# Optimization experiments

Hardware: AMD Instinct MI355X
Metric: run time of the kernel (lower is better)

## Reference

```python
import jax, jax.numpy as jnp
import numpy as np

B, N, D = 16, 1024, 768
H = 12
HD = D // H
HID = 4 * D
EPS = 1e-6


def _layernorm(x, g, b):
    mu = jnp.mean(x, axis=-1, keepdims=True)
    var = jnp.mean(jnp.square(x - mu), axis=-1, keepdims=True)
    return (x - mu) * jax.lax.rsqrt(var + EPS) * g + b


def setup_inputs() -> dict:
    key = jax.random.key(0)
    ks = jax.random.split(key, 8)
    s_d = 1.0 / np.sqrt(D)
    s_h = 1.0 / np.sqrt(HID)
    return {
        "x": jax.random.normal(ks[0], (B, N, D), dtype=jnp.float32),
        "qkv_w": jax.random.uniform(ks[1], (3 * D, D), jnp.float32, -s_d, s_d),
        "proj_w": jax.random.uniform(ks[2], (D, D), jnp.float32, -s_d, s_d),
        "proj_b": jax.random.uniform(ks[3], (D,), jnp.float32, -s_d, s_d),
        "fc1_w": jax.random.uniform(ks[4], (HID, D), jnp.float32, -s_d, s_d),
        "fc1_b": jax.random.uniform(ks[5], (HID,), jnp.float32, -s_d, s_d),
        "fc2_w": jax.random.uniform(ks[6], (D, HID), jnp.float32, -s_h, s_h),
        "fc2_b": jax.random.uniform(ks[7], (D,), jnp.float32, -s_h, s_h),
        "norm1_g": jnp.ones((D,), jnp.float32),
        "norm1_b": jnp.zeros((D,), jnp.float32),
        "norm2_g": jnp.ones((D,), jnp.float32),
        "norm2_b": jnp.zeros((D,), jnp.float32),
    }


def _attention(x, qkv_w, proj_w, proj_b):
    b, n, _ = x.shape
    qkv = x @ qkv_w.T                                  # [b,n,3D] (no bias: qkv_bias=False)
    qkv = qkv.reshape(b, n, 3, H, HD)
    q, k, v = (jnp.transpose(qkv[:, :, i], (0, 2, 1, 3)) for i in range(3))  # [b,h,n,hd]
    scale = HD ** (-0.5)
    dots = jnp.einsum("bhid,bhjd->bhij", q, k) * scale
    attn = jax.nn.softmax(dots, axis=-1)
    out = jnp.einsum("bhij,bhjd->bhid", attn, v)
    out = jnp.transpose(out, (0, 2, 1, 3)).reshape(b, n, H * HD)
    return out @ proj_w.T + proj_b


def _mlp(x, fc1_w, fc1_b, fc2_w, fc2_b):
    h = jax.nn.gelu(x @ fc1_w.T + fc1_b, approximate=False)
    return h @ fc2_w.T + fc2_b


def reference(x, qkv_w, proj_w, proj_b, fc1_w, fc1_b, fc2_w, fc2_b,
              norm1_g, norm1_b, norm2_g, norm2_b):
    x = x + _attention(_layernorm(x, norm1_g, norm1_b), qkv_w, proj_w, proj_b)
    x = x + _mlp(_layernorm(x, norm2_g, norm2_b), fc1_w, fc1_b, fc2_w, fc2_b)
    return x
```

## Files before the change

### kernel.cpp

```cpp
#include <hip/hip_runtime.h>
#include <hip/hip_bf16.h>
#include <math.h>

using bf16 = __hip_bfloat16;
typedef __attribute__((ext_vector_type(8))) short short8;
typedef __attribute__((ext_vector_type(4))) short shortx4;
typedef __attribute__((ext_vector_type(4))) float floatx4;

#define BB 16
#define NN 1024
#define DD 768
#define HH 12
#define HD 64
#define HID 3072

__device__ __forceinline__ floatx4 mfma_bf16(short8 a, short8 b, floatx4 c) {
  return __builtin_amdgcn_mfma_f32_16x16x32_bf16(a, b, c, 0, 0, 0);
}

__device__ __forceinline__ short bf16_bits(float f) {
  union { bf16 h; short s; } u;
  u.h = __float2bfloat16(f);
  return u.s;
}

__device__ __forceinline__ void async_copy16(const void* g, void* l) {
  __builtin_amdgcn_global_load_lds(
      (const __attribute__((address_space(1))) unsigned int*)g,
      (__attribute__((address_space(3))) unsigned int*)l,
      16, 0, 0);
}

__device__ __forceinline__ float gelu_f(float x) {
  const float z = x * fmaf(0.10294324f, x * x, 2.3022082f);
  const float e = exp2f(z);
  return x - x * __builtin_amdgcn_rcpf(e + 1.0f);
}

__global__ __launch_bounds__(256)
void cvt_kernel(const float* __restrict__ in, bf16* __restrict__ out, int n4)
{
  const int i = blockIdx.x * 256 + threadIdx.x;
  if (i >= n4) return;
  const float4 v = ((const float4*)in)[i];
  shortx4 o;
  o.x = bf16_bits(v.x); o.y = bf16_bits(v.y);
  o.z = bf16_bits(v.z); o.w = bf16_bits(v.w);
  ((shortx4*)out)[i] = o;
}

__global__ __launch_bounds__(256)
void ln_kernel(const float* __restrict__ x, const float* __restrict__ g,
               const float* __restrict__ b, bf16* __restrict__ y)
{
  const int row = blockIdx.x;
  const int t = threadIdx.x;
  const float* xr = x + (size_t)row * DD;
  float v[3];
  float s = 0.f, s2 = 0.f;
#pragma unroll
  for (int i = 0; i < 3; ++i) {
    float f = xr[t + i * 256];
    v[i] = f;
    s += f;
    s2 += f * f;
  }
#pragma unroll
  for (int off = 1; off < 64; off <<= 1) {
    s  += __shfl_xor(s, off);
    s2 += __shfl_xor(s2, off);
  }
  __shared__ float red[2][4];
  const int wave = t >> 6, lane = t & 63;
  if (lane == 0) { red[0][wave] = s; red[1][wave] = s2; }
  __syncthreads();
  s  = red[0][0] + red[0][1] + red[0][2] + red[0][3];
  s2 = red[1][0] + red[1][1] + red[1][2] + red[1][3];
  const float mu = s * (1.f / DD);
  const float var = s2 * (1.f / DD) - mu * mu;
  const float inv = rsqrtf(var + 1e-6f);
  bf16* yr = y + (size_t)row * DD;
#pragma unroll
  for (int i = 0; i < 3; ++i) {
    int c = t + i * 256;
    yr[c] = __float2bfloat16((v[i] - mu) * inv * g[c] + b[c]);
  }
}

template <int EPI>
__global__ __launch_bounds__(256, 4)
void gemm_kernel(const bf16* __restrict__ A, const bf16* __restrict__ W,
                 const float* __restrict__ bias, const float* __restrict__ res,
                 void* __restrict__ Cv, int N, int K)
{
  __shared__ __align__(16) short smem[16896];
  short* sA = smem;
  short* sB = smem + 8192;

  const int tid  = threadIdx.x;
  const int lane = tid & 63;
  const int wave = tid >> 6;
  const int wm = wave & 1, wn = wave >> 1;
  const int row16 = lane & 15, quad = lane >> 4;

  const int lin = blockIdx.y * gridDim.x + blockIdx.x;
  const int per = gridDim.x * 8;
  const int pan = lin / per, rem = lin % per;
  const int bm = (pan * 8 + (rem & 7)) * 128;
  const int bn = (rem >> 3) * 128;

  const int lrow = lane >> 3;
  const int lkc  = (lane & 7) ^ lrow;

  const bf16* Ag = A + (size_t)(bm + wave * 32 + lrow) * K + lkc * 8;
  const bf16* Bg = W + (size_t)(bn + wave * 32 + lrow) * K + lkc * 8;
  short* sAw = sA + wave * 2048;
  short* sBw = sB + wave * 2048;

  floatx4 acc[4][4] = {};

  for (int kt = 0; kt < K; kt += 64) {
#pragma unroll
    for (int g = 0; g < 4; ++g) {
      async_copy16(Ag + (size_t)g * 8 * K + kt, sAw + g * 512);
      async_copy16(Bg + (size_t)g * 8 * K + kt, sBw + g * 512);
    }
    __syncthreads();
#pragma unroll
    for (int c = 0; c < 2; ++c) {
      short8 af[4], bfr[4];
      const int kc = c * 4 + quad;
#pragma unroll
      for (int mt = 0; mt < 4; ++mt) {
        const int row = wm * 64 + mt * 16 + row16;
        af[mt] = *(const short8*)&sA[(row >> 3) * 512 + ((row & 7) * 8 + (kc ^ (row & 7))) * 8];
      }
#pragma unroll
      for (int nt = 0; nt < 4; ++nt) {
        const int row = wn * 64 + nt * 16 + row16;
        bfr[nt] = *(const short8*)&sB[(row >> 3) * 512 + ((row & 7) * 8 + (kc ^ (row & 7))) * 8];
      }
#pragma unroll
      for (int mt = 0; mt < 4; ++mt)
#pragma unroll
        for (int nt = 0; nt < 4; ++nt)
          acc[mt][nt] = mfma_bf16(bfr[nt], af[mt], acc[mt][nt]);
    }
    __syncthreads();
  }

  if (EPI == 1) {
#pragma unroll
    for (int mt = 0; mt < 4; ++mt) {
      const int row = bm + wm * 64 + mt * 16 + row16;
#pragma unroll
      for (int nt = 0; nt < 4; ++nt) {
        const int col = bn + wn * 64 + nt * 16 + quad * 4;
        const floatx4 bv = *(const floatx4*)&bias[col];
        const floatx4 rv = *(const floatx4*)&res[(size_t)row * N + col];
        floatx4 o;
#pragma unroll
        for (int r = 0; r < 4; ++r) o[r] = acc[mt][nt][r] + bv[r] + rv[r];
        *(floatx4*)&((float*)Cv)[(size_t)row * N + col] = o;
      }
    }
  } else {
    short* sC = smem;
#pragma unroll
    for (int mt = 0; mt < 4; ++mt) {
      const int lr = wm * 64 + mt * 16 + row16;
#pragma unroll
      for (int nt = 0; nt < 4; ++nt) {
        const int lc = wn * 64 + nt * 16 + quad * 4;
        floatx4 bv = {};
        if (EPI == 2) bv = *(const floatx4*)&bias[bn + lc];
        shortx4 pk;
#pragma unroll
        for (int r = 0; r < 4; ++r) {
          float v = acc[mt][nt][r] + bv[r];
          if (EPI == 2) v = gelu_f(v);
          pk[r] = bf16_bits(v);
        }
        *(shortx4*)&sC[lr * 132 + lc] = pk;
      }
    }
    __syncthreads();
#pragma unroll
    for (int it = 0; it < 8; ++it) {
      const int row = (tid >> 4) + it * 16;
      const int col = (tid & 15) * 8;
      short8 v = *(const short8*)&sC[row * 132 + col];
      *(short8*)&((bf16*)Cv)[(size_t)(bm + row) * N + bn + col] = v;
    }
  }
}

__global__ __launch_bounds__(256)
void vtrans_kernel(const bf16* __restrict__ qkv, bf16* __restrict__ vt)
{
  const int bh = blockIdx.y;
  const int b = bh / HH, h = bh % HH;
  const int n0 = blockIdx.x * 64;
  __shared__ __align__(16) short tile[64 * 72];
  const int tid = threadIdx.x;

  const int r = tid >> 2, c16 = (tid & 3) * 16;
  const bf16* src = qkv + (size_t)(b * NN + n0 + r) * 2304 + 2 * DD + h * 64 + c16;
  *(short8*)&tile[r * 72 + c16]     = *(const short8*)(src);
  *(short8*)&tile[r * 72 + c16 + 8] = *(const short8*)(src + 8);
  __syncthreads();

#pragma unroll
  for (int it = 0; it < 2; ++it) {
    const int d  = (tid >> 3) + it * 32;
    const int jg = (tid & 7) * 8;
    short8 o;
#pragma unroll
    for (int t = 0; t < 8; ++t) ((short*)&o)[t] = tile[(jg + t) * 72 + d];
    *(short8*)&vt[((size_t)bh * 64 + d) * NN + n0 + jg] = o;
  }
}

__global__ __launch_bounds__(256, 2)
void attn_kernel(const bf16* __restrict__ qkv, const bf16* __restrict__ vt,
                 bf16* __restrict__ out)
{
  const int bh = blockIdx.y;
  const int b = bh / HH, h = bh % HH;
  const int q0 = blockIdx.x * 128;
  const int tid = threadIdx.x;
  const int lane = tid & 63;
  const int wave = tid >> 6;
  const int row16 = lane & 15, quad = lane >> 4;

  __shared__ __align__(16) short sK[4096];
  __shared__ __align__(16) short sVt[4096];
  __shared__ __align__(16) short sP[4][2][1024];

  const bf16* base  = qkv + (size_t)b * NN * 2304 + h * 64;
  const bf16* vbase = vt + (size_t)bh * 64 * NN;

  short8 qf[2][2];
#pragma unroll
  for (int qg = 0; qg < 2; ++qg) {
    const bf16* qrow = base + (size_t)(q0 + wave * 32 + qg * 16 + row16) * 2304;
    qf[qg][0] = *(const short8*)(qrow + quad * 8);
    qf[qg][1] = *(const short8*)(qrow + 32 + quad * 8);
  }

  floatx4 o_acc[2][4] = {};
  floatx4 l_acc[2] = {};
  const short8 ones = { (short)0x3F80, (short)0x3F80, (short)0x3F80, (short)0x3F80,
                        (short)0x3F80, (short)0x3F80, (short)0x3F80, (short)0x3F80 };

  const bf16* ksrc = base + DD + (size_t)(wave * 16 + row16) * 2304 + quad * 8;
  const bf16* vsrc = vbase + (size_t)(wave * 16 + row16) * NN + quad * 8;
  short* kdst = sK + wave * 1024 + lane * 8;
  short* vdst = sVt + wave * 1024 + lane * 8;

  async_copy16(ksrc, kdst);
  async_copy16(ksrc + 32, kdst + 512);
  async_copy16(vsrc, vdst);
  async_copy16(vsrc + 32, vdst + 512);

  const float ESC = 0.1803368801f;

  for (int jt = 0; jt < NN / 64; ++jt) {
    __syncthreads();

    short8 vb[4][2];
#pragma unroll
    for (int dt = 0; dt < 4; ++dt) {
      vb[dt][0] = *(const short8*)&sVt[dt * 1024 + lane * 8];
      vb[dt][1] = *(const short8*)&sVt[dt * 1024 + 512 + lane * 8];
    }
    short8 kb[4][2];
#pragma unroll
    for (int nt = 0; nt < 4; ++nt) {
      kb[nt][0] = *(const short8*)&sK[nt * 1024 + lane * 8];
      kb[nt][1] = *(const short8*)&sK[nt * 1024 + 512 + lane * 8];
    }
    __syncthreads();

    if (jt + 1 < NN / 64) {
      const bf16* k2 = ksrc + (size_t)(jt + 1) * 64 * 2304;
      const bf16* v2 = vsrc + (jt + 1) * 64;
      async_copy16(k2, kdst);
      async_copy16(k2 + 32, kdst + 512);
      async_copy16(v2, vdst);
      async_copy16(v2 + 32, vdst + 512);
    }

#pragma unroll
    for (int nt = 0; nt < 4; ++nt) {
#pragma unroll
      for (int qg = 0; qg < 2; ++qg) {
        floatx4 st = {};
        st = mfma_bf16(kb[nt][0], qf[qg][0], st);
        st = mfma_bf16(kb[nt][1], qf[qg][1], st);
        shortx4 pk;
#pragma unroll
        for (int r = 0; r < 4; ++r)
          pk[r] = bf16_bits(exp2f(fminf(st[r] * ESC, 30.f)));
        *(shortx4*)&sP[wave][qg][(row16 + 16 * (2 * nt + (quad >> 1))) * 8 +
                                 (quad & 1) * 4] = pk;
      }
    }

#pragma unroll
    for (int qg = 0; qg < 2; ++qg) {
      const short8 pf0 = *(const short8*)&sP[wave][qg][lane * 8];
      const short8 pf1 = *(const short8*)&sP[wave][qg][512 + lane * 8];
      l_acc[qg] = mfma_bf16(pf0, ones, l_acc[qg]);
      l_acc[qg] = mfma_bf16(pf1, ones, l_acc[qg]);
#pragma unroll
      for (int dt = 0; dt < 4; ++dt) {
        o_acc[qg][dt] = mfma_bf16(pf0, vb[dt][0], o_acc[qg][dt]);
        o_acc[qg][dt] = mfma_bf16(pf1, vb[dt][1], o_acc[qg][dt]);
      }
    }
  }

#pragma unroll
  for (int qg = 0; qg < 2; ++qg) {
#pragma unroll
    for (int r = 0; r < 4; ++r) {
      const float inv = 1.f / l_acc[qg][r];
      const size_t n = (size_t)(b * NN + q0 + wave * 32 + qg * 16 + quad * 4 + r);
#pragma unroll
      for (int dt = 0; dt < 4; ++dt) {
        out[n * DD + h * 64 + dt * 16 + row16] =
            __float2bfloat16(o_acc[qg][dt][r] * inv);
      }
    }
  }
}

extern "C" void kernel_launch(void* const* d_in, const int* in_sizes, int n_in,
                              void* d_out, int out_size, void* d_ws, size_t ws_size,
                              hipStream_t stream)
{
  const float* x       = (const float*)d_in[0];
  const float* qkv_w   = (const float*)d_in[1];
  const float* proj_w  = (const float*)d_in[2];
  const float* proj_b  = (const float*)d_in[3];
  const float* fc1_w   = (const float*)d_in[4];
  const float* fc1_b   = (const float*)d_in[5];
  const float* fc2_w   = (const float*)d_in[6];
  const float* fc2_b   = (const float*)d_in[7];
  const float* norm1_g = (const float*)d_in[8];
  const float* norm1_b = (const float*)d_in[9];
  const float* norm2_g = (const float*)d_in[10];
  const float* norm2_b = (const float*)d_in[11];
  float* out = (float*)d_out;

  const int M = BB * NN;
  char* ws = (char*)d_ws;

  bf16* wq = (bf16*)ws;
  bf16* wp = wq + (size_t)3 * DD * DD;
  bf16* w1 = wp + (size_t)DD * DD;
  bf16* w2 = w1 + (size_t)HID * DD;
  bf16* xn = w2 + (size_t)DD * HID;
  char* p2 = (char*)(xn + (size_t)M * DD);
  const size_t base_b = (size_t)(p2 - ws);

  int NBc = 1;
  for (int c = 16; c >= 1; c >>= 1)
    if (ws_size >= base_b + (size_t)c * 1024 * 7680) { NBc = c; break; }

  const int Rc = NBc * NN;
  bf16* qkvb = (bf16*)p2;
  bf16* aob  = qkvb + (size_t)Rc * 2304;
  bf16* vtb  = aob  + (size_t)Rc * DD;
  bf16* hb   = (bf16*)p2;

  cvt_kernel<<<(3 * DD * DD / 4 + 255) / 256, 256, 0, stream>>>(qkv_w, wq, 3 * DD * DD / 4);
  cvt_kernel<<<(DD * DD / 4 + 255) / 256, 256, 0, stream>>>(proj_w, wp, DD * DD / 4);
  cvt_kernel<<<(HID * DD / 4 + 255) / 256, 256, 0, stream>>>(fc1_w, w1, HID * DD / 4);
  cvt_kernel<<<(DD * HID / 4 + 255) / 256, 256, 0, stream>>>(fc2_w, w2, DD * HID / 4);

  ln_kernel<<<M, 256, 0, stream>>>(x, norm1_g, norm1_b, xn);

  for (int c = 0; c < BB / NBc; ++c) {
    const size_t r0 = (size_t)c * Rc;
    gemm_kernel<0><<<dim3(3 * DD / 128, Rc / 128), 256, 0, stream>>>(
        xn + r0 * DD, wq, nullptr, nullptr, qkvb, 3 * DD, DD);
    vtrans_kernel<<<dim3(NN / 64, NBc * HH), 256, 0, stream>>>(qkvb, vtb);
    attn_kernel<<<dim3(NN / 128, NBc * HH), 256, 0, stream>>>(qkvb, vtb, aob);
    gemm_kernel<1><<<dim3(DD / 128, Rc / 128), 256, 0, stream>>>(
        aob, wp, proj_b, x + r0 * DD, out + r0 * DD, DD, DD);
  }

  ln_kernel<<<M, 256, 0, stream>>>(out, norm2_g, norm2_b, xn);

  for (int c = 0; c < BB / NBc; ++c) {
    const size_t r0 = (size_t)c * Rc;
    gemm_kernel<2><<<dim3(HID / 128, Rc / 128), 256, 0, stream>>>(
        xn + r0 * DD, w1, fc1_b, nullptr, hb, HID, DD);
    gemm_kernel<1><<<dim3(DD / 128, Rc / 128), 256, 0, stream>>>(
        hb, w2, fc2_b, out + r0 * DD, out + r0 * DD, DD, HID);
  }
}
```

Measured before the change: 559.9 us.

## Fold softmax scale into QKV epilogue, remap attention blocks per XCD, pack bf16 converts

```diff
diff --git a/kernel.cpp b/kernel.cpp
--- a/kernel.cpp
+++ b/kernel.cpp
@@ -13,6 +13,8 @@
 #define HH 12
 #define HD 64
 #define HID 3072
+
+#define QSCALE 0.1803368801f
 
 __device__ __forceinline__ floatx4 mfma_bf16(short8 a, short8 b, floatx4 c) {
   return __builtin_amdgcn_mfma_f32_16x16x32_bf16(a, b, c, 0, 0, 0);
@@ -179,6 +181,7 @@
         for (int r = 0; r < 4; ++r) {
           float v = acc[mt][nt][r] + bv[r];
           if (EPI == 2) v = gelu_f(v);
+          if (EPI == 0 && bn + lc < DD) v *= QSCALE;
           pk[r] = bf16_bits(v);
         }
         *(shortx4*)&sC[lr * 132 + lc] = pk;
@@ -225,9 +228,19 @@
 void attn_kernel(const bf16* __restrict__ qkv, const bf16* __restrict__ vt,
                  bf16* __restrict__ out)
 {
-  const int bh = blockIdx.y;
+  const int nbh = gridDim.y;
+  int bh, qi;
+  if ((nbh & 7) == 0) {
+    const int lin = blockIdx.y * 8 + blockIdx.x;
+    const int xcd = lin & 7;
+    const int w   = lin >> 3;
+    bh = xcd * (nbh >> 3) + (w >> 3);
+    qi = w & 7;
+  } else {
+    bh = blockIdx.y; qi = blockIdx.x;
+  }
   const int b = bh / HH, h = bh % HH;
-  const int q0 = blockIdx.x * 128;
+  const int q0 = qi * 128;
   const int tid = threadIdx.x;
   const int lane = tid & 63;
   const int wave = tid >> 6;
@@ -262,8 +275,6 @@
   async_copy16(ksrc + 32, kdst + 512);
   async_copy16(vsrc, vdst);
   async_copy16(vsrc + 32, vdst + 512);
-
-  const float ESC = 0.1803368801f;
 
   for (int jt = 0; jt < NN / 64; ++jt) {
     __syncthreads();
@@ -298,12 +309,15 @@
         floatx4 st = {};
         st = mfma_bf16(kb[nt][0], qf[qg][0], st);
         st = mfma_bf16(kb[nt][1], qf[qg][1], st);
-        shortx4 pk;
-#pragma unroll
-        for (int r = 0; r < 4; ++r)
-          pk[r] = bf16_bits(exp2f(fminf(st[r] * ESC, 30.f)));
+        const float e0 = exp2f(fminf(st[0], 30.f));
+        const float e1 = exp2f(fminf(st[1], 30.f));
+        const float e2 = exp2f(fminf(st[2], 30.f));
+        const float e3 = exp2f(fminf(st[3], 30.f));
+        union { __hip_bfloat162 h2[2]; shortx4 s4; } pu;
+        pu.h2[0] = __float22bfloat162_rn(make_float2(e0, e1));
+        pu.h2[1] = __float22bfloat162_rn(make_float2(e2, e3));
         *(shortx4*)&sP[wave][qg][(row16 + 16 * (2 * nt + (quad >> 1))) * 8 +
-                                 (quad & 1) * 4] = pk;
+                                 (quad & 1) * 4] = pu.s4;
       }
     }
 
```

Result: no change. 558.0 us (-0.3%).
